# Optimization experiments

Measured on AMD Instinct MI355X. Metric: run time of the kernel, lower is better.

## Reference

```python
import jax, jax.numpy as jnp
import numpy as np

B, N_IN, D_IN, N_OUT, D_OUT, ROUTINGS = 512, 1152, 8, 10, 16, 3


def squash(s, axis=-1):
    # scale = |s|^2 / (1 + |s|^2) / (|s| + 1e-8)
    norm = jnp.linalg.norm(s, axis=axis, keepdims=True)
    return (norm ** 2 / (1.0 + norm ** 2) / (norm + 1e-8)) * s


def setup_inputs() -> dict:
    key = jax.random.key(0)
    k1, k2 = jax.random.split(key)
    x = jax.random.normal(k1, (B, N_IN, D_IN), dtype=jnp.float32)
    weight = 0.01 * jax.random.normal(k2, (N_OUT, N_IN, D_OUT, D_IN), dtype=jnp.float32)
    return {"x": x, "weight": weight}


def reference(x, weight):
    # x: [B, N_IN, D_IN]; weight: [N_OUT, N_IN, D_OUT, D_IN]
    # x_hat[b,o,n,:] = weight[o,n] @ x[b,n]  -> [B, N_OUT, N_IN, D_OUT]
    x_hat = jnp.einsum('onij,bnj->boni', weight, x)
    x_hat_det = jax.lax.stop_gradient(x_hat)

    # routing logits b: [B, N_OUT, N_IN]
    b = jnp.zeros(x_hat.shape[:3], dtype=x_hat.dtype)
    outputs = None
    for i in range(ROUTINGS):
        c = jax.nn.softmax(b, axis=1)  # softmax over output capsules
        if i == ROUTINGS - 1:
            outputs = squash(jnp.sum(c[..., None] * x_hat, axis=2))  # [B, N_OUT, D_OUT]
        else:
            outputs = squash(jnp.sum(c[..., None] * x_hat_det, axis=2))
            # agreement: b += <outputs, x_hat_det> over D_OUT
            b = b + jnp.einsum('bod,bond->bon', outputs, x_hat_det)
    return outputs  # [B, N_OUT, D_OUT]
```

## Files before the change

kernel.cpp:

```cpp
#include <hip/hip_runtime.h>
#include <hip/hip_bf16.h>

#define B_    512
#define NI    1152
#define NO    10
#define BT    16
#define NBT   32
#define NC    24
#define NCH   48
#define RNDS  3
#define RN    16

typedef __attribute__((ext_vector_type(8))) short bf16x8;
typedef __attribute__((ext_vector_type(4))) float f32x4;
typedef __attribute__((ext_vector_type(8))) unsigned short u16x8;

#define SPART_F32  ((size_t)NC * NBT * NO * 256)
#define OUTSUM_F32 ((size_t)NBT * NO * 256)
#define XB_US      ((size_t)NBT * NC * RNDS * 2048)
#define WB_US      ((size_t)NC * RNDS * 24576)

__device__ inline unsigned short f2bf(float f) {
    __hip_bfloat16 h = __float2bfloat16(f);
    return *reinterpret_cast<unsigned short*>(&h);
}

__device__ inline void gld_lds16(const void* g, void* lds) {
    __builtin_amdgcn_global_load_lds(
        (const __attribute__((address_space(1))) void*)g,
        (__attribute__((address_space(3))) void*)lds, 16, 0, 0);
}

__global__ __launch_bounds__(256) void cvt_x(
    const float* __restrict__ x, unsigned short* __restrict__ xb)
{
    const int t  = blockIdx.x * 256 + threadIdx.x;
    const int nl = t & 15;
    const int bl = (t >> 4) & 15;
    const int rest = t >> 8;
    const int r  = rest % 3;
    const int bc = rest / 3;
    const int nc = bc % NC, bt = bc / NC;
    const int b  = bt * BT + bl;
    const int n  = nc * NCH + r * RN + nl;
    const float* src = x + ((size_t)b * NI + n) * 8;
    float4 v0 = *reinterpret_cast<const float4*>(src);
    float4 v1 = *reinterpret_cast<const float4*>(src + 4);
    u16x8 u = { f2bf(v0.x), f2bf(v0.y), f2bf(v0.z), f2bf(v0.w),
                f2bf(v1.x), f2bf(v1.y), f2bf(v1.z), f2bf(v1.w) };
    *reinterpret_cast<u16x8*>(xb + (size_t)rest * 2048 + nl * 128 + bl * 8) = u;
}

__global__ __launch_bounds__(256) void cvt_w(
    const float* __restrict__ w, unsigned short* __restrict__ wb)
{
    const int t  = blockIdx.x * 256 + threadIdx.x;
    const int d  = t & 15;
    const int hi = (t >> 4) & 3;
    const int oq = (t >> 6) % 3;
    const int rest = t / 192;
    const int nl = rest % RN;
    const int r  = (rest / RN) % 3;
    const int nc = rest / (RN * 3);
    const int o  = oq * 4 + hi;
    const int n  = nc * NCH + r * RN + nl;
    u16x8 u = {0,0,0,0,0,0,0,0};
    if (o < NO) {
        const float* src = w + ((size_t)o * NI + n) * 128 + d * 8;
        float4 v0 = *reinterpret_cast<const float4*>(src);
        float4 v1 = *reinterpret_cast<const float4*>(src + 4);
        u = (u16x8){ f2bf(v0.x), f2bf(v0.y), f2bf(v0.z), f2bf(v0.w),
                     f2bf(v1.x), f2bf(v1.y), f2bf(v1.z), f2bf(v1.w) };
    }
    *reinterpret_cast<u16x8*>(
        wb + ((size_t)nc * 3 + r) * 24576 + (nl * 3 + oq) * 512
           + (hi * 16 + d) * 8) = u;
}

template<bool UNIFORM>
__global__ __launch_bounds__(256, 3) void caps_iter(
    const unsigned short* __restrict__ xb,
    const unsigned short* __restrict__ wb,
    const float* __restrict__ outsum,
    float* __restrict__ s_part)
{
    __shared__ unsigned short lds[26624];

    const int tid = threadIdx.x;
    const int w   = tid >> 6;
    const int l   = tid & 63;
    const int b16 = l & 15;
    const int hi  = l >> 4;
    const int blk = blockIdx.x;
    const int xcd = blk & 7, idx = blk >> 3;
    const int nc  = xcd * 3 + (idx >> 5);
    const int bt  = idx & 31;

    f32x4 outf[NO];
    if constexpr (!UNIFORM) {
        #pragma unroll
        for (int o = 0; o < NO; ++o)
            outf[o] = *reinterpret_cast<const f32x4*>(
                outsum + (((size_t)bt * NO + o) * 64 + l) * 4);
    }

    f32x4 sacc[NO];
    #pragma unroll
    for (int o = 0; o < NO; ++o) sacc[o] = (f32x4){0.f, 0.f, 0.f, 0.f};

    for (int r = 0; r < RNDS; ++r) {
        if (r) __syncthreads();
        const unsigned short* wsrc = wb + ((size_t)nc * 3 + r) * 24576;
        #pragma unroll
        for (int k = 0; k < 12; ++k)
            gld_lds16(wsrc + (k * 256 + tid) * 8, (char*)lds + (k * 256 + tid) * 16);
        const unsigned short* xsrc = xb + (((size_t)bt * NC + nc) * 3 + r) * 2048;
        gld_lds16(xsrc + tid * 8, (char*)lds + 49152 + tid * 16);
        asm volatile("s_waitcnt vmcnt(0)" ::: "memory");
        __syncthreads();

        #pragma unroll 1
        for (int i = 0; i < 4; ++i) {
            const int nl = w * 4 + i;
            bf16x8 bv = *reinterpret_cast<const bf16x8*>(
                &lds[24576 + nl * 128 + b16 * 8]);
            bf16x8 bvt[4];
            #pragma unroll
            for (int t = 0; t < 4; ++t)
                bvt[t] = (hi == t) ? bv : (bf16x8){0,0,0,0,0,0,0,0};

            if constexpr (UNIFORM) {
                #pragma unroll
                for (int oq = 0; oq < 3; ++oq) {
                    bf16x8 av = *reinterpret_cast<const bf16x8*>(
                        &lds[(nl * 3 + oq) * 512 + l * 8]);
                    const int tmax = (oq < 2) ? 4 : 2;
                    #pragma unroll
                    for (int t = 0; t < tmax; ++t)
                        sacc[oq * 4 + t] = __builtin_amdgcn_mfma_f32_16x16x32_bf16(
                            av, bvt[t], sacc[oq * 4 + t], 0, 0, 0);
                }
            } else {
                float lg[NO];
                #pragma unroll
                for (int oq = 0; oq < 3; ++oq) {
                    bf16x8 av = *reinterpret_cast<const bf16x8*>(
                        &lds[(nl * 3 + oq) * 512 + l * 8]);
                    const int tmax = (oq < 2) ? 4 : 2;
                    #pragma unroll
                    for (int t = 0; t < tmax; ++t) {
                        f32x4 xh = __builtin_amdgcn_mfma_f32_16x16x32_bf16(
                            av, bvt[t], (f32x4){0.f, 0.f, 0.f, 0.f}, 0, 0, 0);
                        const int o = oq * 4 + t;
                        float pp = outf[o][0] * xh[0];
                        pp = fmaf(outf[o][1], xh[1], pp);
                        pp = fmaf(outf[o][2], xh[2], pp);
                        pp = fmaf(outf[o][3], xh[3], pp);
                        pp += __shfl_xor(pp, 16, 64);
                        pp += __shfl_xor(pp, 32, 64);
                        lg[o] = pp;
                    }
                }
                float sum = 0.f;
                #pragma unroll
                for (int o = 0; o < NO; ++o) { lg[o] = __expf(lg[o]); sum += lg[o]; }
                const float rs = __builtin_amdgcn_rcpf(sum);
                #pragma unroll
                for (int oq = 0; oq < 3; ++oq) {
                    bf16x8 av = *reinterpret_cast<const bf16x8*>(
                        &lds[(nl * 3 + oq) * 512 + l * 8]);
                    const int tmax = (oq < 2) ? 4 : 2;
                    #pragma unroll
                    for (int t = 0; t < tmax; ++t) {
                        f32x4 xh = __builtin_amdgcn_mfma_f32_16x16x32_bf16(
                            av, bvt[t], (f32x4){0.f, 0.f, 0.f, 0.f}, 0, 0, 0);
                        const int o = oq * 4 + t;
                        const float cc = lg[o] * rs;
                        sacc[o][0] = fmaf(cc, xh[0], sacc[o][0]);
                        sacc[o][1] = fmaf(cc, xh[1], sacc[o][1]);
                        sacc[o][2] = fmaf(cc, xh[2], sacc[o][2]);
                        sacc[o][3] = fmaf(cc, xh[3], sacc[o][3]);
                    }
                }
            }
        }
    }

    __syncthreads();
    const float sc = UNIFORM ? 0.1f : 1.0f;
    f32x4* red = reinterpret_cast<f32x4*>(lds);
    #pragma unroll
    for (int o = 0; o < NO; ++o)
        red[w * 640 + o * 64 + l] =
            (f32x4){sacc[o][0] * sc, sacc[o][1] * sc,
                    sacc[o][2] * sc, sacc[o][3] * sc};
    __syncthreads();
    float* base = s_part + ((size_t)nc * NBT + bt) * 2560;
    for (int g = tid; g < 640; g += 256) {
        f32x4 a0 = red[g], a1 = red[640 + g], a2 = red[1280 + g], a3 = red[1920 + g];
        f32x4 s;
        #pragma unroll
        for (int q = 0; q < 4; ++q) s[q] = (a0[q] + a1[q]) + (a2[q] + a3[q]);
        *reinterpret_cast<f32x4*>(base + (size_t)g * 4) = s;
    }
}

template<int MODE>
__global__ __launch_bounds__(256) void caps_squash(
    const float* __restrict__ s_part,
    float* __restrict__ outsum,
    float* __restrict__ dout)
{
    __shared__ float sq[256];
    const int bo = blockIdx.x;
    const int t  = threadIdx.x;

    float s = 0.f;
    #pragma unroll
    for (int nc = 0; nc < NC; ++nc)
        s += s_part[((size_t)nc * NBT * NO + bo) * 256 + t];

    float n2 = s * s;
    n2 += __shfl_xor(n2, 1, 64);
    n2 += __shfl_xor(n2, 2, 64);
    sq[t] = n2;
    __syncthreads();
    const int base = t & 63;
    n2 = (sq[base] + sq[64 + base]) + (sq[128 + base] + sq[192 + base]);

    const float norm  = sqrtf(n2);
    const float scale = n2 / ((1.f + n2) * (norm + 1e-8f));
    const float v = scale * s;

    if constexpr (MODE == 0) {
        outsum[(size_t)bo * 256 + t] = v;
    } else if constexpr (MODE == 1) {
        outsum[(size_t)bo * 256 + t] += v;
    } else {
        const int bt = bo / NO, o = bo - bt * NO;
        const int b16 = (t >> 2) & 15, hi = t >> 6, q = t & 3;
        dout[((size_t)(bt * BT + b16) * NO + o) * 16 + hi * 4 + q] = v;
    }
}

extern "C" void kernel_launch(void* const* d_in, const int* in_sizes, int n_in,
                              void* d_out, int out_size, void* d_ws, size_t ws_size,
                              hipStream_t stream) {
    const float* x = (const float*)d_in[0];
    const float* w = (const float*)d_in[1];
    float* out = (float*)d_out;

    float* s_part          = (float*)d_ws;
    float* outsum          = s_part + SPART_F32;
    unsigned short* xb     = (unsigned short*)(outsum + OUTSUM_F32);
    unsigned short* wb     = xb + XB_US;

    cvt_x<<<dim3(2304), dim3(256), 0, stream>>>(x, xb);
    cvt_w<<<dim3(864),  dim3(256), 0, stream>>>(w, wb);

    dim3 gI(NBT * NC), bI(256);
    dim3 gS(NBT * NO), bS(256);

    caps_iter<true ><<<gI, bI, 0, stream>>>(xb, wb, nullptr, s_part);
    caps_squash<0><<<gS, bS, 0, stream>>>(s_part, outsum, nullptr);
    caps_iter<false><<<gI, bI, 0, stream>>>(xb, wb, outsum, s_part);
    caps_squash<1><<<gS, bS, 0, stream>>>(s_part, outsum, nullptr);
    caps_iter<false><<<gI, bI, 0, stream>>>(xb, wb, outsum, s_part);
    caps_squash<2><<<gS, bS, 0, stream>>>(s_part, nullptr, out);
}
```

Measured before the change: 81.99 us.

## Double-buffer LDS staging in caps_iter and merge bf16 conversion kernels

Splits each chunk's 48 input capsules into six rounds of 8 instead of three of 16, and double-buffers LDS so the global-to-LDS load for the next round runs while the current round computes. This hides load latency that was previously exposed by a wait and barrier before every round. The x and w bf16 conversion kernels are merged into one launch, and the staging layouts are simplified to linear stores. LDS use stays about the same, but there are twice as many barriers and each round has less work to cover its load.

```diff
diff --git a/kernel.cpp b/kernel.cpp
--- a/kernel.cpp
+++ b/kernel.cpp
@@ -8,8 +8,11 @@
 #define NBT   32
 #define NC    24
 #define NCH   48
-#define RNDS  3
-#define RN    16
+#define RNDS  6
+#define RN    8
+
+#define WBUF_US 12288
+#define BUF_US  13312
 
 typedef __attribute__((ext_vector_type(8))) short bf16x8;
 typedef __attribute__((ext_vector_type(4))) float f32x4;
@@ -17,8 +20,8 @@
 
 #define SPART_F32  ((size_t)NC * NBT * NO * 256)
 #define OUTSUM_F32 ((size_t)NBT * NO * 256)
-#define XB_US      ((size_t)NBT * NC * RNDS * 2048)
-#define WB_US      ((size_t)NC * RNDS * 24576)
+#define XB_US      ((size_t)NBT * NC * RNDS * 1024)
+#define WB_US      ((size_t)NC * RNDS * WBUF_US)
 
 __device__ inline unsigned short f2bf(float f) {
     __hip_bfloat16 h = __float2bfloat16(f);
@@ -31,50 +34,47 @@
         (__attribute__((address_space(3))) void*)lds, 16, 0, 0);
 }
 
-__global__ __launch_bounds__(256) void cvt_x(
-    const float* __restrict__ x, unsigned short* __restrict__ xb)
+__global__ __launch_bounds__(256) void cvt_xw(
+    const float* __restrict__ x, const float* __restrict__ w,
+    unsigned short* __restrict__ xb, unsigned short* __restrict__ wb)
 {
-    const int t  = blockIdx.x * 256 + threadIdx.x;
-    const int nl = t & 15;
-    const int bl = (t >> 4) & 15;
-    const int rest = t >> 8;
-    const int r  = rest % 3;
-    const int bc = rest / 3;
-    const int nc = bc % NC, bt = bc / NC;
-    const int b  = bt * BT + bl;
-    const int n  = nc * NCH + r * RN + nl;
-    const float* src = x + ((size_t)b * NI + n) * 8;
-    float4 v0 = *reinterpret_cast<const float4*>(src);
-    float4 v1 = *reinterpret_cast<const float4*>(src + 4);
-    u16x8 u = { f2bf(v0.x), f2bf(v0.y), f2bf(v0.z), f2bf(v0.w),
-                f2bf(v1.x), f2bf(v1.y), f2bf(v1.z), f2bf(v1.w) };
-    *reinterpret_cast<u16x8*>(xb + (size_t)rest * 2048 + nl * 128 + bl * 8) = u;
-}
-
-__global__ __launch_bounds__(256) void cvt_w(
-    const float* __restrict__ w, unsigned short* __restrict__ wb)
-{
-    const int t  = blockIdx.x * 256 + threadIdx.x;
-    const int d  = t & 15;
-    const int hi = (t >> 4) & 3;
-    const int oq = (t >> 6) % 3;
-    const int rest = t / 192;
-    const int nl = rest % RN;
-    const int r  = (rest / RN) % 3;
-    const int nc = rest / (RN * 3);
-    const int o  = oq * 4 + hi;
-    const int n  = nc * NCH + r * RN + nl;
-    u16x8 u = {0,0,0,0,0,0,0,0};
-    if (o < NO) {
-        const float* src = w + ((size_t)o * NI + n) * 128 + d * 8;
+    const int blk = blockIdx.x;
+    if (blk < 2304) {
+        const int t   = blk * 256 + threadIdx.x;
+        const int m   = t & 127;
+        const int img = t >> 7;
+        const int nl  = m >> 4, bl = m & 15;
+        const int r   = img % RNDS;
+        const int bc  = img / RNDS;
+        const int nc  = bc % NC, bt = bc / NC;
+        const int b   = bt * BT + bl;
+        const int n   = nc * NCH + r * RN + nl;
+        const float* src = x + ((size_t)b * NI + n) * 8;
         float4 v0 = *reinterpret_cast<const float4*>(src);
         float4 v1 = *reinterpret_cast<const float4*>(src + 4);
-        u = (u16x8){ f2bf(v0.x), f2bf(v0.y), f2bf(v0.z), f2bf(v0.w),
-                     f2bf(v1.x), f2bf(v1.y), f2bf(v1.z), f2bf(v1.w) };
-    }
-    *reinterpret_cast<u16x8*>(
-        wb + ((size_t)nc * 3 + r) * 24576 + (nl * 3 + oq) * 512
-           + (hi * 16 + d) * 8) = u;
+        u16x8 u = { f2bf(v0.x), f2bf(v0.y), f2bf(v0.z), f2bf(v0.w),
+                    f2bf(v1.x), f2bf(v1.y), f2bf(v1.z), f2bf(v1.w) };
+        *reinterpret_cast<u16x8*>(xb + (size_t)t * 8) = u;
+    } else {
+        const int t    = (blk - 2304) * 256 + threadIdx.x;
+        const int lane = t & 63;
+        const int gs   = (t >> 6) % 24;
+        const int img  = t / 1536;
+        const int hi   = lane >> 4, d = lane & 15;
+        const int nl   = gs / 3, oq = gs % 3;
+        const int r    = img % RNDS, nc = img / RNDS;
+        const int o    = oq * 4 + hi;
+        const int n    = nc * NCH + r * RN + nl;
+        u16x8 u = {0,0,0,0,0,0,0,0};
+        if (o < NO) {
+            const float* src = w + ((size_t)o * NI + n) * 128 + d * 8;
+            float4 v0 = *reinterpret_cast<const float4*>(src);
+            float4 v1 = *reinterpret_cast<const float4*>(src + 4);
+            u = (u16x8){ f2bf(v0.x), f2bf(v0.y), f2bf(v0.z), f2bf(v0.w),
+                         f2bf(v1.x), f2bf(v1.y), f2bf(v1.z), f2bf(v1.w) };
+        }
+        *reinterpret_cast<u16x8*>(wb + (size_t)t * 8) = u;
+    }
 }
 
 template<bool UNIFORM>
@@ -84,7 +84,7 @@
     const float* __restrict__ outsum,
     float* __restrict__ s_part)
 {
-    __shared__ unsigned short lds[26624];
+    __shared__ unsigned short lds[2 * BUF_US];
 
     const int tid = threadIdx.x;
     const int w   = tid >> 6;
@@ -96,6 +96,20 @@
     const int nc  = xcd * 3 + (idx >> 5);
     const int bt  = idx & 31;
 
+    const unsigned short* wsrc = wb + (size_t)nc * (RNDS * WBUF_US);
+    const unsigned short* xsrc = xb + ((size_t)bt * NC + nc) * (RNDS * 1024);
+
+    auto stage = [&](int r, int kbuf) {
+        const unsigned short* wr = wsrc + (size_t)r * WBUF_US;
+        char* dst = (char*)lds + kbuf * (BUF_US * 2);
+        #pragma unroll
+        for (int k = 0; k < 6; ++k)
+            gld_lds16(wr + (k * 256 + tid) * 8, dst + (k * 256 + tid) * 16);
+        if (tid < 128)
+            gld_lds16(xsrc + (size_t)r * 1024 + tid * 8,
+                      dst + WBUF_US * 2 + tid * 16);
+    };
+
     f32x4 outf[NO];
     if constexpr (!UNIFORM) {
         #pragma unroll
@@ -108,22 +122,21 @@
     #pragma unroll
     for (int o = 0; o < NO; ++o) sacc[o] = (f32x4){0.f, 0.f, 0.f, 0.f};
 
+    stage(0, 0);
+    asm volatile("s_waitcnt vmcnt(0)" ::: "memory");
+    __syncthreads();
+
+    #pragma unroll 1
     for (int r = 0; r < RNDS; ++r) {
-        if (r) __syncthreads();
-        const unsigned short* wsrc = wb + ((size_t)nc * 3 + r) * 24576;
-        #pragma unroll
-        for (int k = 0; k < 12; ++k)
-            gld_lds16(wsrc + (k * 256 + tid) * 8, (char*)lds + (k * 256 + tid) * 16);
-        const unsigned short* xsrc = xb + (((size_t)bt * NC + nc) * 3 + r) * 2048;
-        gld_lds16(xsrc + tid * 8, (char*)lds + 49152 + tid * 16);
-        asm volatile("s_waitcnt vmcnt(0)" ::: "memory");
-        __syncthreads();
+        if (r + 1 < RNDS) stage(r + 1, (r + 1) & 1);
+
+        const int ub = (r & 1) * BUF_US;
 
         #pragma unroll 1
-        for (int i = 0; i < 4; ++i) {
-            const int nl = w * 4 + i;
+        for (int i = 0; i < 2; ++i) {
+            const int nl = w * 2 + i;
             bf16x8 bv = *reinterpret_cast<const bf16x8*>(
-                &lds[24576 + nl * 128 + b16 * 8]);
+                &lds[ub + WBUF_US + nl * 128 + b16 * 8]);
             bf16x8 bvt[4];
             #pragma unroll
             for (int t = 0; t < 4; ++t)
@@ -133,7 +146,7 @@
                 #pragma unroll
                 for (int oq = 0; oq < 3; ++oq) {
                     bf16x8 av = *reinterpret_cast<const bf16x8*>(
-                        &lds[(nl * 3 + oq) * 512 + l * 8]);
+                        &lds[ub + (nl * 3 + oq) * 512 + l * 8]);
                     const int tmax = (oq < 2) ? 4 : 2;
                     #pragma unroll
                     for (int t = 0; t < tmax; ++t)
@@ -145,7 +158,7 @@
                 #pragma unroll
                 for (int oq = 0; oq < 3; ++oq) {
                     bf16x8 av = *reinterpret_cast<const bf16x8*>(
-                        &lds[(nl * 3 + oq) * 512 + l * 8]);
+                        &lds[ub + (nl * 3 + oq) * 512 + l * 8]);
                     const int tmax = (oq < 2) ? 4 : 2;
                     #pragma unroll
                     for (int t = 0; t < tmax; ++t) {
@@ -168,7 +181,7 @@
                 #pragma unroll
                 for (int oq = 0; oq < 3; ++oq) {
                     bf16x8 av = *reinterpret_cast<const bf16x8*>(
-                        &lds[(nl * 3 + oq) * 512 + l * 8]);
+                        &lds[ub + (nl * 3 + oq) * 512 + l * 8]);
                     const int tmax = (oq < 2) ? 4 : 2;
                     #pragma unroll
                     for (int t = 0; t < tmax; ++t) {
@@ -184,9 +197,11 @@
                 }
             }
         }
-    }
-
-    __syncthreads();
+
+        asm volatile("s_waitcnt vmcnt(0)" ::: "memory");
+        __syncthreads();
+    }
+
     const float sc = UNIFORM ? 0.1f : 1.0f;
     f32x4* red = reinterpret_cast<f32x4*>(lds);
     #pragma unroll
@@ -255,8 +270,7 @@
     unsigned short* xb     = (unsigned short*)(outsum + OUTSUM_F32);
     unsigned short* wb     = xb + XB_US;
 
-    cvt_x<<<dim3(2304), dim3(256), 0, stream>>>(x, xb);
-    cvt_w<<<dim3(864),  dim3(256), 0, stream>>>(w, wb);
+    cvt_xw<<<dim3(3168), dim3(256), 0, stream>>>(x, w, xb, wb);
 
     dim3 gI(NBT * NC), bI(256);
     dim3 gS(NBT * NO), bS(256);
```

New measurement: 77.91 us. 1.05x faster.
